# Kernel tuning notes

Measured on AMD Instinct MI355X. Metric: run time of the kernel, lower is better.

Reference implementation:

```python
import jax, jax.numpy as jnp
import numpy as np

INPUT_SIZE = 2
EMB = 64
RNN = 128
EDGE_RNN = 128
OUT = 5
N = 500000


def setup_inputs() -> dict:
    key = jax.random.key(0)
    ks = jax.random.split(key, 12)
    s = 0.1
    return {
        "pos": jax.random.normal(ks[0], (N, INPUT_SIZE), jnp.float32),
        "h_other": jax.random.normal(ks[1], (N, 2 * EDGE_RNN), jnp.float32),
        "h": jax.random.normal(ks[2], (N, RNN), jnp.float32),
        "enc_W": jax.random.normal(ks[3], (EMB, INPUT_SIZE), jnp.float32) * s,
        "enc_b": jnp.zeros((EMB,), jnp.float32),
        "henc_W": jax.random.normal(ks[4], (EMB, 2 * EDGE_RNN), jnp.float32) * s,
        "henc_b": jnp.zeros((EMB,), jnp.float32),
        "W_ih": jax.random.normal(ks[5], (3 * RNN, 2 * EMB), jnp.float32) * s,
        "b_ih": jax.random.normal(ks[6], (3 * RNN,), jnp.float32) * s,
        "W_hh": jax.random.normal(ks[7], (3 * RNN, RNN), jnp.float32) * s,
        "b_hh": jax.random.normal(ks[8], (3 * RNN,), jnp.float32) * s,
        "dec_W": jax.random.normal(ks[9], (OUT, RNN), jnp.float32) * s,
        "dec_b": jnp.zeros((OUT,), jnp.float32),
    }


def reference(pos, h_other, h, enc_W, enc_b, henc_W, henc_b,
              W_ih, b_ih, W_hh, b_hh, dec_W, dec_b):
    # encode position and edge-RNN hidden states
    enc_in = jax.nn.relu(pos @ enc_W.T + enc_b)          # [N, EMB]
    enc_hid = jax.nn.relu(h_other @ henc_W.T + henc_b)   # [N, EMB]
    x = jnp.concatenate([enc_in, enc_hid], axis=1)       # [N, 2*EMB]
    # GRUCell (torch gate order: reset, update, new)
    gx = x @ W_ih.T + b_ih                               # [N, 3*RNN]
    gh = h @ W_hh.T + b_hh                               # [N, 3*RNN]
    xr, xz, xn = jnp.split(gx, 3, axis=1)
    hr, hz, hn = jnp.split(gh, 3, axis=1)
    r = jax.nn.sigmoid(xr + hr)
    z = jax.nn.sigmoid(xz + hz)
    n = jnp.tanh(xn + r * hn)
    h_new = (1.0 - z) * n + z * h                        # [N, RNN]
    out = h_new @ dec_W.T + dec_b                        # [N, OUT]
    return (out, h_new)
```

## Files before the change

kernel.cpp:

```cpp
#include <hip/hip_runtime.h>
#include <hip/hip_bf16.h>

typedef __bf16 bf16x8 __attribute__((ext_vector_type(8)));
typedef float f32x4 __attribute__((ext_vector_type(4)));

#define LDS_HO 0
#define LDS_X  32768
#define LDS_H  49152

#define WS_WIH 0
#define WS_WHH 49152
#define WS_HENC 98304
#define WS_DEC 114688
#define WS_TOTAL 116736

__device__ __forceinline__ unsigned short f2bf(float f) {
    unsigned u = __float_as_uint(f);
    unsigned r = (u + 0x7FFFu + ((u >> 16) & 1u)) >> 16;
    return (unsigned short)r;
}

__device__ __forceinline__ float sigmf(float x) { return 1.0f / (1.0f + __expf(-x)); }
__device__ __forceinline__ float tanh_fast(float x) {
    float t = __expf(-2.0f * fabsf(x));
    float r = (1.0f - t) / (1.0f + t);
    return copysignf(r, x);
}

__global__ void convert_weights_kernel(const float* __restrict__ wih,
                                       const float* __restrict__ whh,
                                       const float* __restrict__ henc,
                                       const float* __restrict__ dec,
                                       unsigned short* __restrict__ ws) {
    int i = blockIdx.x * 256 + threadIdx.x;
    if (i >= WS_TOTAL) return;
    float v;
    if (i < WS_WHH)        v = wih[i];
    else if (i < WS_HENC)  v = whh[i - WS_WHH];
    else if (i < WS_DEC)   v = henc[i - WS_HENC];
    else { int d = i - WS_DEC; v = (d < 640) ? dec[d] : 0.0f; }
    ws[i] = f2bf(v);
}

__launch_bounds__(256, 2)
__global__ void fused_rnn_kernel(const float* __restrict__ pos,
                                 const float* __restrict__ h_other,
                                 const float* __restrict__ h,
                                 const float* __restrict__ enc_W,
                                 const float* __restrict__ enc_b,
                                 const float* __restrict__ henc_b,
                                 const float* __restrict__ b_ih,
                                 const float* __restrict__ b_hh,
                                 const float* __restrict__ dec_b,
                                 const unsigned short* __restrict__ ws,
                                 float* __restrict__ out,
                                 float* __restrict__ hnew,
                                 int N) {
    __shared__ char sm[65536];
    const int tid = threadIdx.x;
    const int w   = tid >> 6;
    const int l   = tid & 63;
    const int lg  = l >> 4;
    const int ln  = l & 15;
    const int row0 = blockIdx.x * 64;

    #pragma unroll
    for (int j = 0; j < 16; ++j) {
        int e0  = (tid + 256 * j) * 4;
        int row = e0 >> 8;
        int col = e0 & 255;
        int grow = row0 + row; if (grow > N - 1) grow = N - 1;
        float4 v = *reinterpret_cast<const float4*>(h_other + (size_t)grow * 256 + col);
        uint2 p;
        p.x = (unsigned)f2bf(v.x) | ((unsigned)f2bf(v.y) << 16);
        p.y = (unsigned)f2bf(v.z) | ((unsigned)f2bf(v.w) << 16);
        int boff = LDS_HO + row * 512 + ((col * 2) ^ ((row & 7) << 4));
        *reinterpret_cast<uint2*>(sm + boff) = p;
    }
    #pragma unroll
    for (int j = 0; j < 8; ++j) {
        int e0  = (tid + 256 * j) * 4;
        int row = e0 >> 7;
        int col = e0 & 127;
        int grow = row0 + row; if (grow > N - 1) grow = N - 1;
        float4 v = *reinterpret_cast<const float4*>(h + (size_t)grow * 128 + col);
        uint2 p;
        p.x = (unsigned)f2bf(v.x) | ((unsigned)f2bf(v.y) << 16);
        p.y = (unsigned)f2bf(v.z) | ((unsigned)f2bf(v.w) << 16);
        int boff = LDS_H + row * 256 + ((col * 2) ^ ((row & 7) << 4));
        *reinterpret_cast<uint2*>(sm + boff) = p;
    }
    {
        int row = tid >> 2;
        int c0  = (tid & 3) * 16;
        int grow = row0 + row; if (grow > N - 1) grow = N - 1;
        float p0 = pos[(size_t)grow * 2 + 0];
        float p1 = pos[(size_t)grow * 2 + 1];
        #pragma unroll
        for (int q = 0; q < 8; ++q) {
            int c = c0 + q * 2;
            float v0 = fmaxf(p0 * enc_W[c * 2]     + p1 * enc_W[c * 2 + 1]  + enc_b[c], 0.f);
            float v1 = fmaxf(p0 * enc_W[c * 2 + 2] + p1 * enc_W[c * 2 + 3]  + enc_b[c + 1], 0.f);
            unsigned pk = (unsigned)f2bf(v0) | ((unsigned)f2bf(v1) << 16);
            int boff = LDS_X + row * 256 + ((c * 2) ^ ((row & 7) << 4));
            *reinterpret_cast<unsigned*>(sm + boff) = pk;
        }
    }
    __syncthreads();

    {
        f32x4 acc[4];
        #pragma unroll
        for (int mt = 0; mt < 4; ++mt) acc[mt] = (f32x4){0.f, 0.f, 0.f, 0.f};
        #pragma unroll
        for (int ks = 0; ks < 8; ++ks) {
            bf16x8 af[4];
            #pragma unroll
            for (int mt = 0; mt < 4; ++mt) {
                int row = mt * 16 + ln;
                int boff = LDS_HO + row * 512 + ((ks * 64 + lg * 16) ^ ((row & 7) << 4));
                af[mt] = *reinterpret_cast<const bf16x8*>(sm + boff);
            }
            const unsigned short* bp = ws + WS_HENC + (size_t)(16 * w + ln) * 256 + ks * 32 + lg * 8;
            bf16x8 bf = *reinterpret_cast<const bf16x8*>(bp);
            #pragma unroll
            for (int mt = 0; mt < 4; ++mt)
                acc[mt] = __builtin_amdgcn_mfma_f32_16x16x32_bf16(af[mt], bf, acc[mt], 0, 0, 0);
        }
        int col = 16 * w + ln;
        float bias = henc_b[col];
        #pragma unroll
        for (int mt = 0; mt < 4; ++mt) {
            #pragma unroll
            for (int i = 0; i < 4; ++i) {
                int row = mt * 16 + lg * 4 + i;
                float v = fmaxf(acc[mt][i] + bias, 0.f);
                int boff = LDS_X + row * 256 + (((64 + col) * 2) ^ ((row & 7) << 4));
                *reinterpret_cast<unsigned short*>(sm + boff) = f2bf(v);
            }
        }
    }
    __syncthreads();

    {
        f32x4 acc[4][8];
        #pragma unroll
        for (int a = 0; a < 4; ++a)
            #pragma unroll
            for (int b = 0; b < 8; ++b) acc[a][b] = (f32x4){0.f, 0.f, 0.f, 0.f};

        const unsigned short* WIH = ws + WS_WIH;
        const unsigned short* WHH = ws + WS_WHH;

        #pragma unroll
        for (int ks = 0; ks < 8; ++ks) {
            const int xbase = (ks < 4) ? LDS_X : LDS_H;
            const int kb = (ks & 3) * 64 + lg * 16;
            bf16x8 af[4];
            #pragma unroll
            for (int mt = 0; mt < 4; ++mt) {
                int row = mt * 16 + ln;
                af[mt] = *reinterpret_cast<const bf16x8*>(sm + xbase + row * 256 + (kb ^ ((row & 7) << 4)));
            }
            const int kk = (ks & 3) * 32 + lg * 8;

            #define MFMA_JOB(job, Wptr, ob) { \
                bf16x8 bfr = *reinterpret_cast<const bf16x8*>((Wptr) + (size_t)((ob) + ln) * 128 + kk); \
                acc[0][job] = __builtin_amdgcn_mfma_f32_16x16x32_bf16(af[0], bfr, acc[0][job], 0, 0, 0); \
                acc[1][job] = __builtin_amdgcn_mfma_f32_16x16x32_bf16(af[1], bfr, acc[1][job], 0, 0, 0); \
                acc[2][job] = __builtin_amdgcn_mfma_f32_16x16x32_bf16(af[2], bfr, acc[2][job], 0, 0, 0); \
                acc[3][job] = __builtin_amdgcn_mfma_f32_16x16x32_bf16(af[3], bfr, acc[3][job], 0, 0, 0); }

            if (ks < 4) {
                MFMA_JOB(0, WIH, 32 * w);
                MFMA_JOB(1, WIH, 32 * w + 16);
                MFMA_JOB(2, WIH, 128 + 32 * w);
                MFMA_JOB(3, WIH, 144 + 32 * w);
                MFMA_JOB(4, WIH, 256 + 32 * w);
                MFMA_JOB(5, WIH, 272 + 32 * w);
            } else {
                MFMA_JOB(0, WHH, 32 * w);
                MFMA_JOB(1, WHH, 32 * w + 16);
                MFMA_JOB(2, WHH, 128 + 32 * w);
                MFMA_JOB(3, WHH, 144 + 32 * w);
                MFMA_JOB(6, WHH, 256 + 32 * w);
                MFMA_JOB(7, WHH, 272 + 32 * w);
            }
            #undef MFMA_JOB
        }

        #pragma unroll
        for (int jt = 0; jt < 2; ++jt) {
            int j = 32 * w + 16 * jt + ln;
            float br  = b_ih[j] + b_hh[j];
            float bz  = b_ih[128 + j] + b_hh[128 + j];
            float bxn = b_ih[256 + j];
            float bhn = b_hh[256 + j];
            #pragma unroll
            for (int mt = 0; mt < 4; ++mt) {
                #pragma unroll
                for (int i = 0; i < 4; ++i) {
                    int row = mt * 16 + lg * 4 + i;
                    int grow = row0 + row;
                    int lrow = (grow < N) ? grow : (N - 1);
                    float r  = sigmf(acc[mt][jt][i] + br);
                    float z  = sigmf(acc[mt][2 + jt][i] + bz);
                    float xn = acc[mt][4 + jt][i] + bxn;
                    float hn = acc[mt][6 + jt][i] + bhn;
                    float nn = tanh_fast(xn + r * hn);
                    float hp = h[(size_t)lrow * 128 + j];
                    float hv = (1.0f - z) * nn + z * hp;
                    if (grow < N) hnew[(size_t)grow * 128 + j] = hv;
                    int boff = LDS_HO + row * 256 + ((j * 2) ^ ((row & 7) << 4));
                    *reinterpret_cast<unsigned short*>(sm + boff) = f2bf(hv);
                }
            }
        }
    }
    __syncthreads();

    {
        f32x4 acc = (f32x4){0.f, 0.f, 0.f, 0.f};
        const unsigned short* DEC = ws + WS_DEC;
        #pragma unroll
        for (int ks = 0; ks < 4; ++ks) {
            int row = w * 16 + ln;
            bf16x8 af = *reinterpret_cast<const bf16x8*>(
                sm + LDS_HO + row * 256 + ((ks * 64 + lg * 16) ^ ((row & 7) << 4)));
            bf16x8 bf = *reinterpret_cast<const bf16x8*>(DEC + (size_t)ln * 128 + ks * 32 + lg * 8);
            acc = __builtin_amdgcn_mfma_f32_16x16x32_bf16(af, bf, acc, 0, 0, 0);
        }
        if (ln < 5) {
            float bias = dec_b[ln];
            #pragma unroll
            for (int i = 0; i < 4; ++i) {
                int grow = row0 + w * 16 + lg * 4 + i;
                if (grow < N) out[(size_t)grow * 5 + ln] = acc[i] + bias;
            }
        }
    }
}

extern "C" void kernel_launch(void* const* d_in, const int* in_sizes, int n_in,
                              void* d_out, int out_size, void* d_ws, size_t ws_size,
                              hipStream_t stream) {
    const float* pos     = (const float*)d_in[0];
    const float* h_other = (const float*)d_in[1];
    const float* h       = (const float*)d_in[2];
    const float* enc_W   = (const float*)d_in[3];
    const float* enc_b   = (const float*)d_in[4];
    const float* henc_W  = (const float*)d_in[5];
    const float* henc_b  = (const float*)d_in[6];
    const float* W_ih    = (const float*)d_in[7];
    const float* b_ih    = (const float*)d_in[8];
    const float* W_hh    = (const float*)d_in[9];
    const float* b_hh    = (const float*)d_in[10];
    const float* dec_W   = (const float*)d_in[11];
    const float* dec_b   = (const float*)d_in[12];

    int N = in_sizes[0] / 2;
    unsigned short* ws = (unsigned short*)d_ws;
    float* out  = (float*)d_out;
    float* hnew = out + (size_t)N * 5;

    hipLaunchKernelGGL(convert_weights_kernel, dim3((WS_TOTAL + 255) / 256), dim3(256), 0, stream,
                       W_ih, W_hh, henc_W, dec_W, ws);
    int blocks = (N + 63) / 64;
    hipLaunchKernelGGL(fused_rnn_kernel, dim3(blocks), dim3(256), 0, stream,
                       pos, h_other, h, enc_W, enc_b, henc_b, b_ih, b_hh, dec_b,
                       ws, out, hnew, N);
}
```

Before: 476.5 us.

## Split fused GRU block across 8 waves, use packed bf16 convert and fast rcp

```diff
diff --git a/kernel.cpp b/kernel.cpp
--- a/kernel.cpp
+++ b/kernel.cpp
@@ -20,10 +20,17 @@
     return (unsigned short)r;
 }
 
-__device__ __forceinline__ float sigmf(float x) { return 1.0f / (1.0f + __expf(-x)); }
+__device__ __forceinline__ unsigned cvt_pk_bf16(float a, float b) {
+    unsigned r;
+    asm("v_cvt_pk_bf16_f32 %0, %1, %2" : "=v"(r) : "v"(a), "v"(b));
+    return r;
+}
+
+__device__ __forceinline__ float fast_rcp(float x) { return __builtin_amdgcn_rcpf(x); }
+__device__ __forceinline__ float sigmf(float x) { return fast_rcp(1.0f + __expf(-x)); }
 __device__ __forceinline__ float tanh_fast(float x) {
     float t = __expf(-2.0f * fabsf(x));
-    float r = (1.0f - t) / (1.0f + t);
+    float r = (1.0f - t) * fast_rcp(1.0f + t);
     return copysignf(r, x);
 }
 
@@ -42,7 +49,7 @@
     ws[i] = f2bf(v);
 }
 
-__launch_bounds__(256, 2)
+__launch_bounds__(512, 4)
 __global__ void fused_rnn_kernel(const float* __restrict__ pos,
                                  const float* __restrict__ h_other,
                                  const float* __restrict__ h,
@@ -59,49 +66,51 @@
     __shared__ char sm[65536];
     const int tid = threadIdx.x;
     const int w   = tid >> 6;
+    const int wm  = w >> 2;
+    const int wc  = w & 3;
     const int l   = tid & 63;
     const int lg  = l >> 4;
     const int ln  = l & 15;
     const int row0 = blockIdx.x * 64;
 
     #pragma unroll
-    for (int j = 0; j < 16; ++j) {
-        int e0  = (tid + 256 * j) * 4;
+    for (int j = 0; j < 8; ++j) {
+        int e0  = (tid + 512 * j) * 4;
         int row = e0 >> 8;
         int col = e0 & 255;
         int grow = row0 + row; if (grow > N - 1) grow = N - 1;
         float4 v = *reinterpret_cast<const float4*>(h_other + (size_t)grow * 256 + col);
         uint2 p;
-        p.x = (unsigned)f2bf(v.x) | ((unsigned)f2bf(v.y) << 16);
-        p.y = (unsigned)f2bf(v.z) | ((unsigned)f2bf(v.w) << 16);
+        p.x = cvt_pk_bf16(v.x, v.y);
+        p.y = cvt_pk_bf16(v.z, v.w);
         int boff = LDS_HO + row * 512 + ((col * 2) ^ ((row & 7) << 4));
         *reinterpret_cast<uint2*>(sm + boff) = p;
     }
     #pragma unroll
-    for (int j = 0; j < 8; ++j) {
-        int e0  = (tid + 256 * j) * 4;
+    for (int j = 0; j < 4; ++j) {
+        int e0  = (tid + 512 * j) * 4;
         int row = e0 >> 7;
         int col = e0 & 127;
         int grow = row0 + row; if (grow > N - 1) grow = N - 1;
         float4 v = *reinterpret_cast<const float4*>(h + (size_t)grow * 128 + col);
         uint2 p;
-        p.x = (unsigned)f2bf(v.x) | ((unsigned)f2bf(v.y) << 16);
-        p.y = (unsigned)f2bf(v.z) | ((unsigned)f2bf(v.w) << 16);
+        p.x = cvt_pk_bf16(v.x, v.y);
+        p.y = cvt_pk_bf16(v.z, v.w);
         int boff = LDS_H + row * 256 + ((col * 2) ^ ((row & 7) << 4));
         *reinterpret_cast<uint2*>(sm + boff) = p;
     }
     {
-        int row = tid >> 2;
-        int c0  = (tid & 3) * 16;
+        int row = tid >> 3;
+        int c0  = (tid & 7) * 8;
         int grow = row0 + row; if (grow > N - 1) grow = N - 1;
         float p0 = pos[(size_t)grow * 2 + 0];
         float p1 = pos[(size_t)grow * 2 + 1];
         #pragma unroll
-        for (int q = 0; q < 8; ++q) {
+        for (int q = 0; q < 4; ++q) {
             int c = c0 + q * 2;
             float v0 = fmaxf(p0 * enc_W[c * 2]     + p1 * enc_W[c * 2 + 1]  + enc_b[c], 0.f);
             float v1 = fmaxf(p0 * enc_W[c * 2 + 2] + p1 * enc_W[c * 2 + 3]  + enc_b[c + 1], 0.f);
-            unsigned pk = (unsigned)f2bf(v0) | ((unsigned)f2bf(v1) << 16);
+            unsigned pk = cvt_pk_bf16(v0, v1);
             int boff = LDS_X + row * 256 + ((c * 2) ^ ((row & 7) << 4));
             *reinterpret_cast<unsigned*>(sm + boff) = pk;
         }
@@ -109,31 +118,31 @@
     __syncthreads();
 
     {
-        f32x4 acc[4];
-        #pragma unroll
-        for (int mt = 0; mt < 4; ++mt) acc[mt] = (f32x4){0.f, 0.f, 0.f, 0.f};
+        f32x4 acc[2];
+        #pragma unroll
+        for (int mt = 0; mt < 2; ++mt) acc[mt] = (f32x4){0.f, 0.f, 0.f, 0.f};
         #pragma unroll
         for (int ks = 0; ks < 8; ++ks) {
-            bf16x8 af[4];
-            #pragma unroll
-            for (int mt = 0; mt < 4; ++mt) {
-                int row = mt * 16 + ln;
+            bf16x8 af[2];
+            #pragma unroll
+            for (int mt = 0; mt < 2; ++mt) {
+                int row = 32 * wm + mt * 16 + ln;
                 int boff = LDS_HO + row * 512 + ((ks * 64 + lg * 16) ^ ((row & 7) << 4));
                 af[mt] = *reinterpret_cast<const bf16x8*>(sm + boff);
             }
-            const unsigned short* bp = ws + WS_HENC + (size_t)(16 * w + ln) * 256 + ks * 32 + lg * 8;
+            const unsigned short* bp = ws + WS_HENC + (size_t)(16 * wc + ln) * 256 + ks * 32 + lg * 8;
             bf16x8 bf = *reinterpret_cast<const bf16x8*>(bp);
             #pragma unroll
-            for (int mt = 0; mt < 4; ++mt)
+            for (int mt = 0; mt < 2; ++mt)
                 acc[mt] = __builtin_amdgcn_mfma_f32_16x16x32_bf16(af[mt], bf, acc[mt], 0, 0, 0);
         }
-        int col = 16 * w + ln;
+        int col = 16 * wc + ln;
         float bias = henc_b[col];
         #pragma unroll
-        for (int mt = 0; mt < 4; ++mt) {
+        for (int mt = 0; mt < 2; ++mt) {
             #pragma unroll
             for (int i = 0; i < 4; ++i) {
-                int row = mt * 16 + lg * 4 + i;
+                int row = 32 * wm + mt * 16 + lg * 4 + i;
                 float v = fmaxf(acc[mt][i] + bias, 0.f);
                 int boff = LDS_X + row * 256 + (((64 + col) * 2) ^ ((row & 7) << 4));
                 *reinterpret_cast<unsigned short*>(sm + boff) = f2bf(v);
@@ -143,9 +152,9 @@
     __syncthreads();
 
     {
-        f32x4 acc[4][8];
-        #pragma unroll
-        for (int a = 0; a < 4; ++a)
+        f32x4 acc[2][8];
+        #pragma unroll
+        for (int a = 0; a < 2; ++a)
             #pragma unroll
             for (int b = 0; b < 8; ++b) acc[a][b] = (f32x4){0.f, 0.f, 0.f, 0.f};
 
@@ -156,10 +165,10 @@
         for (int ks = 0; ks < 8; ++ks) {
             const int xbase = (ks < 4) ? LDS_X : LDS_H;
             const int kb = (ks & 3) * 64 + lg * 16;
-            bf16x8 af[4];
-            #pragma unroll
-            for (int mt = 0; mt < 4; ++mt) {
-                int row = mt * 16 + ln;
+            bf16x8 af[2];
+            #pragma unroll
+            for (int mt = 0; mt < 2; ++mt) {
+                int row = 32 * wm + mt * 16 + ln;
                 af[mt] = *reinterpret_cast<const bf16x8*>(sm + xbase + row * 256 + (kb ^ ((row & 7) << 4)));
             }
             const int kk = (ks & 3) * 32 + lg * 8;
@@ -167,40 +176,38 @@
             #define MFMA_JOB(job, Wptr, ob) { \
                 bf16x8 bfr = *reinterpret_cast<const bf16x8*>((Wptr) + (size_t)((ob) + ln) * 128 + kk); \
                 acc[0][job] = __builtin_amdgcn_mfma_f32_16x16x32_bf16(af[0], bfr, acc[0][job], 0, 0, 0); \
-                acc[1][job] = __builtin_amdgcn_mfma_f32_16x16x32_bf16(af[1], bfr, acc[1][job], 0, 0, 0); \
-                acc[2][job] = __builtin_amdgcn_mfma_f32_16x16x32_bf16(af[2], bfr, acc[2][job], 0, 0, 0); \
-                acc[3][job] = __builtin_amdgcn_mfma_f32_16x16x32_bf16(af[3], bfr, acc[3][job], 0, 0, 0); }
+                acc[1][job] = __builtin_amdgcn_mfma_f32_16x16x32_bf16(af[1], bfr, acc[1][job], 0, 0, 0); }
 
             if (ks < 4) {
-                MFMA_JOB(0, WIH, 32 * w);
-                MFMA_JOB(1, WIH, 32 * w + 16);
-                MFMA_JOB(2, WIH, 128 + 32 * w);
-                MFMA_JOB(3, WIH, 144 + 32 * w);
-                MFMA_JOB(4, WIH, 256 + 32 * w);
-                MFMA_JOB(5, WIH, 272 + 32 * w);
+                MFMA_JOB(0, WIH, 32 * wc);
+                MFMA_JOB(1, WIH, 32 * wc + 16);
+                MFMA_JOB(2, WIH, 128 + 32 * wc);
+                MFMA_JOB(3, WIH, 144 + 32 * wc);
+                MFMA_JOB(4, WIH, 256 + 32 * wc);
+                MFMA_JOB(5, WIH, 272 + 32 * wc);
             } else {
-                MFMA_JOB(0, WHH, 32 * w);
-                MFMA_JOB(1, WHH, 32 * w + 16);
-                MFMA_JOB(2, WHH, 128 + 32 * w);
-                MFMA_JOB(3, WHH, 144 + 32 * w);
-                MFMA_JOB(6, WHH, 256 + 32 * w);
-                MFMA_JOB(7, WHH, 272 + 32 * w);
+                MFMA_JOB(0, WHH, 32 * wc);
+                MFMA_JOB(1, WHH, 32 * wc + 16);
+                MFMA_JOB(2, WHH, 128 + 32 * wc);
+                MFMA_JOB(3, WHH, 144 + 32 * wc);
+                MFMA_JOB(6, WHH, 256 + 32 * wc);
+                MFMA_JOB(7, WHH, 272 + 32 * wc);
             }
             #undef MFMA_JOB
         }
 
         #pragma unroll
         for (int jt = 0; jt < 2; ++jt) {
-            int j = 32 * w + 16 * jt + ln;
+            int j = 32 * wc + 16 * jt + ln;
             float br  = b_ih[j] + b_hh[j];
             float bz  = b_ih[128 + j] + b_hh[128 + j];
             float bxn = b_ih[256 + j];
             float bhn = b_hh[256 + j];
             #pragma unroll
-            for (int mt = 0; mt < 4; ++mt) {
+            for (int mt = 0; mt < 2; ++mt) {
                 #pragma unroll
                 for (int i = 0; i < 4; ++i) {
-                    int row = mt * 16 + lg * 4 + i;
+                    int row = 32 * wm + mt * 16 + lg * 4 + i;
                     int grow = row0 + row;
                     int lrow = (grow < N) ? grow : (N - 1);
                     float r  = sigmf(acc[mt][jt][i] + br);
@@ -219,7 +226,7 @@
     }
     __syncthreads();
 
-    {
+    if (w < 4) {
         f32x4 acc = (f32x4){0.f, 0.f, 0.f, 0.f};
         const unsigned short* DEC = ws + WS_DEC;
         #pragma unroll
@@ -266,7 +273,7 @@
     hipLaunchKernelGGL(convert_weights_kernel, dim3((WS_TOTAL + 255) / 256), dim3(256), 0, stream,
                        W_ih, W_hh, henc_W, dec_W, ws);
     int blocks = (N + 63) / 64;
-    hipLaunchKernelGGL(fused_rnn_kernel, dim3(blocks), dim3(256), 0, stream,
+    hipLaunchKernelGGL(fused_rnn_kernel, dim3(blocks), dim3(512), 0, stream,
                        pos, h_other, h, enc_W, enc_b, henc_b, b_ih, b_hh, dec_b,
                        ws, out, hnew, N);
 }
```

Result: slower. 637.6 us (+33.8%).

## Stage gate weights through double-buffered LDS and stream h_other directly into MFMA

Applied to the files above, without the earlier changes.

```diff
diff --git a/kernel.cpp b/kernel.cpp
--- a/kernel.cpp
+++ b/kernel.cpp
@@ -1,18 +1,20 @@
 #include <hip/hip_runtime.h>
 #include <hip/hip_bf16.h>
+#include <stdint.h>
 
 typedef __bf16 bf16x8 __attribute__((ext_vector_type(8)));
 typedef float f32x4 __attribute__((ext_vector_type(4)));
 
-#define LDS_HO 0
-#define LDS_X  32768
-#define LDS_H  49152
-
-#define WS_WIH 0
-#define WS_WHH 49152
-#define WS_HENC 98304
-#define WS_DEC 114688
+#define C_HENC 0
+#define C_GATE 16384
+#define C_DEC  114688
 #define WS_TOTAL 116736
+
+#define LDS_X  0
+#define LDS_H  16384
+#define LDS_W0 32768
+#define LDS_W1 57344
+#define LDS_SZ 81920
 
 __device__ __forceinline__ unsigned short f2bf(float f) {
     unsigned u = __float_as_uint(f);
@@ -20,11 +22,23 @@
     return (unsigned short)r;
 }
 
-__device__ __forceinline__ float sigmf(float x) { return 1.0f / (1.0f + __expf(-x)); }
+__device__ __forceinline__ unsigned cvt_pk_bf16(float a, float b) {
+    unsigned r;
+    asm("v_cvt_pk_bf16_f32 %0, %1, %2" : "=v"(r) : "v"(a), "v"(b));
+    return r;
+}
+
+__device__ __forceinline__ float fast_rcp(float x) { return __builtin_amdgcn_rcpf(x); }
+__device__ __forceinline__ float sigmf(float x) { return fast_rcp(1.0f + __expf(-x)); }
 __device__ __forceinline__ float tanh_fast(float x) {
     float t = __expf(-2.0f * fabsf(x));
-    float r = (1.0f - t) / (1.0f + t);
+    float r = (1.0f - t) * fast_rcp(1.0f + t);
     return copysignf(r, x);
+}
+
+__device__ __forceinline__ int chunk_swz(int lin) {
+    int brow = lin >> 6;
+    return (brow << 6) + ((lin & 63) ^ (((brow >> 1) & 3) << 4));
 }
 
 __global__ void convert_weights_kernel(const float* __restrict__ wih,
@@ -35,10 +49,21 @@
     int i = blockIdx.x * 256 + threadIdx.x;
     if (i >= WS_TOTAL) return;
     float v;
-    if (i < WS_WHH)        v = wih[i];
-    else if (i < WS_HENC)  v = whh[i - WS_WHH];
-    else if (i < WS_DEC)   v = henc[i - WS_HENC];
-    else { int d = i - WS_DEC; v = (d < 640) ? dec[d] : 0.0f; }
+    if (i < C_GATE) {
+        v = henc[i];
+    } else if (i < C_DEC) {
+        int j = i - C_GATE;
+        int t = j / 12288;
+        int r2 = j % 12288;
+        int row = r2 >> 5;
+        int k = r2 & 31;
+        v = (t < 4) ? wih[row * 128 + t * 32 + k]
+                    : whh[row * 128 + (t - 4) * 32 + k];
+    } else {
+        int j = i - C_DEC;
+        int row = j >> 7, k = j & 127;
+        v = (row < 5) ? dec[row * 128 + k] : 0.0f;
+    }
     ws[i] = f2bf(v);
 }
 
@@ -56,26 +81,21 @@
                                  float* __restrict__ out,
                                  float* __restrict__ hnew,
                                  int N) {
-    __shared__ char sm[65536];
+    __shared__ char sm[LDS_SZ];
     const int tid = threadIdx.x;
     const int w   = tid >> 6;
     const int l   = tid & 63;
     const int lg  = l >> 4;
     const int ln  = l & 15;
     const int row0 = blockIdx.x * 64;
-
-    #pragma unroll
-    for (int j = 0; j < 16; ++j) {
-        int e0  = (tid + 256 * j) * 4;
-        int row = e0 >> 8;
-        int col = e0 & 255;
-        int grow = row0 + row; if (grow > N - 1) grow = N - 1;
-        float4 v = *reinterpret_cast<const float4*>(h_other + (size_t)grow * 256 + col);
-        uint2 p;
-        p.x = (unsigned)f2bf(v.x) | ((unsigned)f2bf(v.y) << 16);
-        p.y = (unsigned)f2bf(v.z) | ((unsigned)f2bf(v.w) << 16);
-        int boff = LDS_HO + row * 512 + ((col * 2) ^ ((row & 7) << 4));
-        *reinterpret_cast<uint2*>(sm + boff) = p;
+    const char* wsb = (const char*)ws;
+
+    uint4 st[6];
+    {
+        const char* src = wsb + (size_t)C_GATE * 2;
+        #pragma unroll
+        for (int it = 0; it < 6; ++it)
+            st[it] = *reinterpret_cast<const uint4*>(src + it * 4096 + tid * 16);
     }
     #pragma unroll
     for (int j = 0; j < 8; ++j) {
@@ -85,8 +105,8 @@
         int grow = row0 + row; if (grow > N - 1) grow = N - 1;
         float4 v = *reinterpret_cast<const float4*>(h + (size_t)grow * 128 + col);
         uint2 p;
-        p.x = (unsigned)f2bf(v.x) | ((unsigned)f2bf(v.y) << 16);
-        p.y = (unsigned)f2bf(v.z) | ((unsigned)f2bf(v.w) << 16);
+        p.x = cvt_pk_bf16(v.x, v.y);
+        p.y = cvt_pk_bf16(v.z, v.w);
         int boff = LDS_H + row * 256 + ((col * 2) ^ ((row & 7) << 4));
         *reinterpret_cast<uint2*>(sm + boff) = p;
     }
@@ -99,143 +119,161 @@
         #pragma unroll
         for (int q = 0; q < 8; ++q) {
             int c = c0 + q * 2;
-            float v0 = fmaxf(p0 * enc_W[c * 2]     + p1 * enc_W[c * 2 + 1]  + enc_b[c], 0.f);
-            float v1 = fmaxf(p0 * enc_W[c * 2 + 2] + p1 * enc_W[c * 2 + 3]  + enc_b[c + 1], 0.f);
-            unsigned pk = (unsigned)f2bf(v0) | ((unsigned)f2bf(v1) << 16);
+            float v0 = fmaxf(p0 * enc_W[c * 2]     + p1 * enc_W[c * 2 + 1] + enc_b[c], 0.f);
+            float v1 = fmaxf(p0 * enc_W[c * 2 + 2] + p1 * enc_W[c * 2 + 3] + enc_b[c + 1], 0.f);
+            unsigned pk = cvt_pk_bf16(v0, v1);
             int boff = LDS_X + row * 256 + ((c * 2) ^ ((row & 7) << 4));
             *reinterpret_cast<unsigned*>(sm + boff) = pk;
         }
     }
+    #pragma unroll
+    for (int it = 0; it < 6; ++it) {
+        int lin = it * 4096 + tid * 16;
+        *reinterpret_cast<uint4*>(sm + LDS_W0 + chunk_swz(lin)) = st[it];
+    }
     __syncthreads();
 
     {
-        f32x4 acc[4];
-        #pragma unroll
-        for (int mt = 0; mt < 4; ++mt) acc[mt] = (f32x4){0.f, 0.f, 0.f, 0.f};
-        #pragma unroll
-        for (int ks = 0; ks < 8; ++ks) {
-            bf16x8 af[4];
-            #pragma unroll
-            for (int mt = 0; mt < 4; ++mt) {
-                int row = mt * 16 + ln;
-                int boff = LDS_HO + row * 512 + ((ks * 64 + lg * 16) ^ ((row & 7) << 4));
-                af[mt] = *reinterpret_cast<const bf16x8*>(sm + boff);
-            }
-            const unsigned short* bp = ws + WS_HENC + (size_t)(16 * w + ln) * 256 + ks * 32 + lg * 8;
-            bf16x8 bf = *reinterpret_cast<const bf16x8*>(bp);
-            #pragma unroll
-            for (int mt = 0; mt < 4; ++mt)
-                acc[mt] = __builtin_amdgcn_mfma_f32_16x16x32_bf16(af[mt], bf, acc[mt], 0, 0, 0);
+        bf16x8 Bh[8];
+        const unsigned short* hb = ws + C_HENC + (size_t)(16 * w + ln) * 256;
+        #pragma unroll
+        for (int ks = 0; ks < 8; ++ks)
+            Bh[ks] = *reinterpret_cast<const bf16x8*>(hb + ks * 32 + lg * 8);
+
+        f32x4 e2[4];
+        #pragma unroll
+        for (int mt = 0; mt < 4; ++mt) e2[mt] = (f32x4){0.f, 0.f, 0.f, 0.f};
+        #pragma unroll
+        for (int mt = 0; mt < 4; ++mt) {
+            int grow = row0 + 16 * mt + ln; if (grow > N - 1) grow = N - 1;
+            const float* rp = h_other + (size_t)grow * 256 + lg * 8;
+            #pragma unroll
+            for (int ks = 0; ks < 8; ++ks) {
+                const float* ap = rp + ks * 32;
+                float4 a0 = *reinterpret_cast<const float4*>(ap);
+                float4 a1 = *reinterpret_cast<const float4*>(ap + 4);
+                union { unsigned u[4]; bf16x8 b; } af;
+                af.u[0] = cvt_pk_bf16(a0.x, a0.y);
+                af.u[1] = cvt_pk_bf16(a0.z, a0.w);
+                af.u[2] = cvt_pk_bf16(a1.x, a1.y);
+                af.u[3] = cvt_pk_bf16(a1.z, a1.w);
+                e2[mt] = __builtin_amdgcn_mfma_f32_16x16x32_bf16(af.b, Bh[ks], e2[mt], 0, 0, 0);
+            }
         }
         int col = 16 * w + ln;
         float bias = henc_b[col];
         #pragma unroll
+        for (int mt = 0; mt < 4; ++mt)
+            #pragma unroll
+            for (int i = 0; i < 4; ++i) {
+                int row = 16 * mt + lg * 4 + i;
+                float v = fmaxf(e2[mt][i] + bias, 0.f);
+                *reinterpret_cast<unsigned short*>(
+                    sm + LDS_X + row * 256 + (((64 + col) * 2) ^ ((row & 7) << 4))) = f2bf(v);
+            }
+    }
+    __syncthreads();
+
+    f32x4 acc[4][8];
+    #pragma unroll
+    for (int a = 0; a < 4; ++a)
+        #pragma unroll
+        for (int b = 0; b < 8; ++b) acc[a][b] = (f32x4){0.f, 0.f, 0.f, 0.f};
+
+    #pragma unroll
+    for (int t = 0; t < 8; ++t) {
+        const int wb    = (t & 1) ? LDS_W1 : LDS_W0;
+        const int wbn   = (t & 1) ? LDS_W0 : LDS_W1;
+        const int abase = (t < 4) ? LDS_X : LDS_H;
+        const int kb    = (t & 3) * 64;
+        uint4 cs[6];
+        if (t < 7) {
+            const char* src = wsb + (size_t)(C_GATE + (t + 1) * 12288) * 2;
+            #pragma unroll
+            for (int it = 0; it < 6; ++it)
+                cs[it] = *reinterpret_cast<const uint4*>(src + it * 4096 + tid * 16);
+        }
+        bf16x8 Bf[6];
+        #pragma unroll
+        for (int g = 0; g < 3; ++g)
+            #pragma unroll
+            for (int jt = 0; jt < 2; ++jt) {
+                int brow = g * 128 + 32 * w + 16 * jt + ln;
+                Bf[g * 2 + jt] = *reinterpret_cast<const bf16x8*>(
+                    sm + wb + brow * 64 + (lg * 16 ^ (((brow >> 1) & 3) << 4)));
+            }
+        bf16x8 Af[4];
+        const int swl = (ln & 7) << 4;
+        #pragma unroll
         for (int mt = 0; mt < 4; ++mt) {
+            int row = 16 * mt + ln;
+            Af[mt] = *reinterpret_cast<const bf16x8*>(
+                sm + abase + row * 256 + ((kb + lg * 16) ^ swl));
+        }
+        const int nidx = (t < 4) ? 4 : 6;
+        #pragma unroll
+        for (int mt = 0; mt < 4; ++mt) {
+            acc[mt][0]        = __builtin_amdgcn_mfma_f32_16x16x32_bf16(Af[mt], Bf[0], acc[mt][0], 0, 0, 0);
+            acc[mt][1]        = __builtin_amdgcn_mfma_f32_16x16x32_bf16(Af[mt], Bf[1], acc[mt][1], 0, 0, 0);
+            acc[mt][2]        = __builtin_amdgcn_mfma_f32_16x16x32_bf16(Af[mt], Bf[2], acc[mt][2], 0, 0, 0);
+            acc[mt][3]        = __builtin_amdgcn_mfma_f32_16x16x32_bf16(Af[mt], Bf[3], acc[mt][3], 0, 0, 0);
+            acc[mt][nidx]     = __builtin_amdgcn_mfma_f32_16x16x32_bf16(Af[mt], Bf[4], acc[mt][nidx], 0, 0, 0);
+            acc[mt][nidx + 1] = __builtin_amdgcn_mfma_f32_16x16x32_bf16(Af[mt], Bf[5], acc[mt][nidx + 1], 0, 0, 0);
+        }
+        if (t < 7) {
+            #pragma unroll
+            for (int it = 0; it < 6; ++it) {
+                int lin = it * 4096 + tid * 16;
+                *reinterpret_cast<uint4*>(sm + wbn + chunk_swz(lin)) = cs[it];
+            }
+        }
+        __syncthreads();
+    }
+
+    #pragma unroll
+    for (int jt = 0; jt < 2; ++jt) {
+        int j = 32 * w + 16 * jt + ln;
+        float br  = b_ih[j] + b_hh[j];
+        float bz  = b_ih[128 + j] + b_hh[128 + j];
+        float bxn = b_ih[256 + j];
+        float bhn = b_hh[256 + j];
+        #pragma unroll
+        for (int mt = 0; mt < 4; ++mt)
             #pragma unroll
             for (int i = 0; i < 4; ++i) {
                 int row = mt * 16 + lg * 4 + i;
-                float v = fmaxf(acc[mt][i] + bias, 0.f);
-                int boff = LDS_X + row * 256 + (((64 + col) * 2) ^ ((row & 7) << 4));
-                *reinterpret_cast<unsigned short*>(sm + boff) = f2bf(v);
-            }
-        }
+                int grow = row0 + row;
+                int lrow = (grow < N) ? grow : (N - 1);
+                float r  = sigmf(acc[mt][jt][i] + br);
+                float z  = sigmf(acc[mt][2 + jt][i] + bz);
+                float xn = acc[mt][4 + jt][i] + bxn;
+                float hn = acc[mt][6 + jt][i] + bhn;
+                float nn = tanh_fast(xn + r * hn);
+                float hp = h[(size_t)lrow * 128 + j];
+                float hv = (1.0f - z) * nn + z * hp;
+                if (grow < N) hnew[(size_t)grow * 128 + j] = hv;
+                *reinterpret_cast<unsigned short*>(
+                    sm + LDS_X + row * 256 + ((j * 2) ^ ((row & 7) << 4))) = f2bf(hv);
+            }
     }
     __syncthreads();
 
     {
-        f32x4 acc[4][8];
-        #pragma unroll
-        for (int a = 0; a < 4; ++a)
-            #pragma unroll
-            for (int b = 0; b < 8; ++b) acc[a][b] = (f32x4){0.f, 0.f, 0.f, 0.f};
-
-        const unsigned short* WIH = ws + WS_WIH;
-        const unsigned short* WHH = ws + WS_WHH;
-
-        #pragma unroll
-        for (int ks = 0; ks < 8; ++ks) {
-            const int xbase = (ks < 4) ? LDS_X : LDS_H;
-            const int kb = (ks & 3) * 64 + lg * 16;
-            bf16x8 af[4];
-            #pragma unroll
-            for (int mt = 0; mt < 4; ++mt) {
-                int row = mt * 16 + ln;
-                af[mt] = *reinterpret_cast<const bf16x8*>(sm + xbase + row * 256 + (kb ^ ((row & 7) << 4)));
-            }
-            const int kk = (ks & 3) * 32 + lg * 8;
-
-            #define MFMA_JOB(job, Wptr, ob) { \
-                bf16x8 bfr = *reinterpret_cast<const bf16x8*>((Wptr) + (size_t)((ob) + ln) * 128 + kk); \
-                acc[0][job] = __builtin_amdgcn_mfma_f32_16x16x32_bf16(af[0], bfr, acc[0][job], 0, 0, 0); \
-                acc[1][job] = __builtin_amdgcn_mfma_f32_16x16x32_bf16(af[1], bfr, acc[1][job], 0, 0, 0); \
-                acc[2][job] = __builtin_amdgcn_mfma_f32_16x16x32_bf16(af[2], bfr, acc[2][job], 0, 0, 0); \
-                acc[3][job] = __builtin_amdgcn_mfma_f32_16x16x32_bf16(af[3], bfr, acc[3][job], 0, 0, 0); }
-
-            if (ks < 4) {
-                MFMA_JOB(0, WIH, 32 * w);
-                MFMA_JOB(1, WIH, 32 * w + 16);
-                MFMA_JOB(2, WIH, 128 + 32 * w);
-                MFMA_JOB(3, WIH, 144 + 32 * w);
-                MFMA_JOB(4, WIH, 256 + 32 * w);
-                MFMA_JOB(5, WIH, 272 + 32 * w);
-            } else {
-                MFMA_JOB(0, WHH, 32 * w);
-                MFMA_JOB(1, WHH, 32 * w + 16);
-                MFMA_JOB(2, WHH, 128 + 32 * w);
-                MFMA_JOB(3, WHH, 144 + 32 * w);
-                MFMA_JOB(6, WHH, 256 + 32 * w);
-                MFMA_JOB(7, WHH, 272 + 32 * w);
-            }
-            #undef MFMA_JOB
-        }
-
-        #pragma unroll
-        for (int jt = 0; jt < 2; ++jt) {
-            int j = 32 * w + 16 * jt + ln;
-            float br  = b_ih[j] + b_hh[j];
-            float bz  = b_ih[128 + j] + b_hh[128 + j];
-            float bxn = b_ih[256 + j];
-            float bhn = b_hh[256 + j];
-            #pragma unroll
-            for (int mt = 0; mt < 4; ++mt) {
-                #pragma unroll
-                for (int i = 0; i < 4; ++i) {
-                    int row = mt * 16 + lg * 4 + i;
-                    int grow = row0 + row;
-                    int lrow = (grow < N) ? grow : (N - 1);
-                    float r  = sigmf(acc[mt][jt][i] + br);
-                    float z  = sigmf(acc[mt][2 + jt][i] + bz);
-                    float xn = acc[mt][4 + jt][i] + bxn;
-                    float hn = acc[mt][6 + jt][i] + bhn;
-                    float nn = tanh_fast(xn + r * hn);
-                    float hp = h[(size_t)lrow * 128 + j];
-                    float hv = (1.0f - z) * nn + z * hp;
-                    if (grow < N) hnew[(size_t)grow * 128 + j] = hv;
-                    int boff = LDS_HO + row * 256 + ((j * 2) ^ ((row & 7) << 4));
-                    *reinterpret_cast<unsigned short*>(sm + boff) = f2bf(hv);
-                }
-            }
-        }
-    }
-    __syncthreads();
-
-    {
-        f32x4 acc = (f32x4){0.f, 0.f, 0.f, 0.f};
-        const unsigned short* DEC = ws + WS_DEC;
+        f32x4 oc = (f32x4){0.f, 0.f, 0.f, 0.f};
         #pragma unroll
         for (int ks = 0; ks < 4; ++ks) {
-            int row = w * 16 + ln;
+            int row = 16 * w + ln;
             bf16x8 af = *reinterpret_cast<const bf16x8*>(
-                sm + LDS_HO + row * 256 + ((ks * 64 + lg * 16) ^ ((row & 7) << 4)));
-            bf16x8 bf = *reinterpret_cast<const bf16x8*>(DEC + (size_t)ln * 128 + ks * 32 + lg * 8);
-            acc = __builtin_amdgcn_mfma_f32_16x16x32_bf16(af, bf, acc, 0, 0, 0);
+                sm + LDS_X + row * 256 + ((ks * 64 + lg * 16) ^ ((row & 7) << 4)));
+            bf16x8 bf = *reinterpret_cast<const bf16x8*>(ws + C_DEC + ln * 128 + ks * 32 + lg * 8);
+            oc = __builtin_amdgcn_mfma_f32_16x16x32_bf16(af, bf, oc, 0, 0, 0);
         }
         if (ln < 5) {
             float bias = dec_b[ln];
             #pragma unroll
             for (int i = 0; i < 4; ++i) {
-                int grow = row0 + w * 16 + lg * 4 + i;
-                if (grow < N) out[(size_t)grow * 5 + ln] = acc[i] + bias;
+                int grow = row0 + 16 * w + lg * 4 + i;
+                if (grow < N) out[(size_t)grow * 5 + ln] = oc[i] + bias;
             }
         }
     }
```

Result: slower. 536.8 us (+12.6%).
